# Kernel tuning notes

Hardware: AMD Instinct MI355X
Metric: run time of the kernel (lower is better)

The kernel has to match this reference:

```python
import jax, jax.numpy as jnp
import numpy as np

DIM = 1024
NUM_HEADS = 16
HEAD_DIM = DIM // NUM_HEADS
SCALE = HEAD_DIM ** -0.5


def setup_inputs() -> dict:
    key = jax.random.key(0)
    ks = jax.random.split(key, 7)
    b, n = 2, 2048
    x = jax.random.normal(ks[0], (b, n, DIM), dtype=jnp.float32)
    s = DIM ** -0.5
    Wq = jax.random.normal(ks[1], (DIM, DIM), dtype=jnp.float32) * s
    bq = jax.random.normal(ks[2], (DIM,), dtype=jnp.float32) * 0.01
    Wk = jax.random.normal(ks[3], (DIM, DIM), dtype=jnp.float32) * s
    bk = jax.random.normal(ks[4], (DIM,), dtype=jnp.float32) * 0.01
    Wv = jax.random.normal(ks[5], (DIM, DIM), dtype=jnp.float32) * s
    bv = jax.random.normal(ks[6], (DIM,), dtype=jnp.float32) * 0.01
    return {"x": x, "Wq": Wq, "bq": bq, "Wk": Wk, "bk": bk, "Wv": Wv, "bv": bv}


def reference(x, Wq, bq, Wk, bk, Wv, bv):
    b, n, _ = x.shape
    # Linear projections (torch Linear: x @ W.T + b; here W stored as [in, out])
    q = x @ Wq + bq
    k = x @ Wk + bk
    v = x @ Wv + bv
    # split heads: [b, n, h*d] -> [b, h, n, d]
    split = lambda t: t.reshape(b, n, NUM_HEADS, HEAD_DIM).transpose(0, 2, 1, 3)
    q, k, v = split(q), split(k), split(v)
    sim = jnp.einsum('bhid,bhjd->bhij', q, k) * SCALE
    attn = jax.nn.softmax(sim, axis=-1)
    out = jnp.einsum('bhij,bhjd->bhid', attn, v)
    return out.transpose(0, 2, 1, 3).reshape(b, n, DIM)
```

## Files before the change

kernel.cpp:

```cpp
#include <hip/hip_runtime.h>
#include <cstdint>
#include <cstddef>

#define NB    2
#define SEQ   2048
#define DIMC  1024
#define NH    16
#define HDIM  64
#define MROWS (NB*SEQ)
#define NFEAT (3*DIMC)
#define KVBLK 64

typedef _Float16 half8 __attribute__((ext_vector_type(8)));
typedef _Float16 half4 __attribute__((ext_vector_type(4)));
typedef _Float16 half2v __attribute__((ext_vector_type(2)));
typedef __fp16   fp16x2 __attribute__((ext_vector_type(2)));
typedef float    f32x4 __attribute__((ext_vector_type(4)));

typedef const __attribute__((address_space(1))) void* gas_ptr;
typedef __attribute__((address_space(3))) void*       las_ptr;

__device__ __forceinline__ void gload_lds16(const void* g, void* l) {
    __builtin_amdgcn_global_load_lds((gas_ptr)g, (las_ptr)l, 16, 0, 0);
}

__device__ __forceinline__ float fast_exp2(float x) {
    float r;
    asm("v_exp_f32 %0, %1" : "=v"(r) : "v"(x));
    return r;
}

__device__ __forceinline__ half2v pk_f16(float a, float b) {
    fp16x2 r = __builtin_amdgcn_cvt_pkrtz(a, b);
    return __builtin_bit_cast(half2v, r);
}

__global__ __launch_bounds__(256) void k_prep(const float* __restrict__ x,
                                              const float* __restrict__ Wq,
                                              const float* __restrict__ Wk,
                                              const float* __restrict__ Wv,
                                              _Float16* __restrict__ x16,
                                              _Float16* __restrict__ wt) {
    __shared__ float tile[64][65];
    const int tid = threadIdx.x;
    if (blockIdx.x < 4096) {
        int i = (blockIdx.x * 256 + tid) * 4;
        float4 v = *reinterpret_cast<const float4*>(x + i);
        half4 h = { (_Float16)v.x, (_Float16)v.y, (_Float16)v.z, (_Float16)v.w };
        *reinterpret_cast<half4*>(x16 + i) = h;
        return;
    }
    const int bid  = blockIdx.x - 4096;
    const int midx = bid >> 8;
    const int t2   = bid & 255;
    const int i0   = (t2 >> 4) * 64;
    const int o0   = (t2 & 15) * 64;
    const float* W = (midx == 0) ? Wq : (midx == 1 ? Wk : Wv);
    #pragma unroll
    for (int p = 0; p < 4; ++p) {
        int id = p * 256 + tid;
        int r = id >> 4, c4 = (id & 15) * 4;
        float4 v = *reinterpret_cast<const float4*>(W + (size_t)(i0 + r) * DIMC + o0 + c4);
        tile[r][c4 + 0] = v.x; tile[r][c4 + 1] = v.y;
        tile[r][c4 + 2] = v.z; tile[r][c4 + 3] = v.w;
    }
    __syncthreads();
    #pragma unroll
    for (int p = 0; p < 4; ++p) {
        int id = p * 256 + tid;
        int oc = id >> 4, i4 = (id & 15) * 4;
        half4 h = { (_Float16)tile[i4 + 0][oc], (_Float16)tile[i4 + 1][oc],
                    (_Float16)tile[i4 + 2][oc], (_Float16)tile[i4 + 3][oc] };
        *reinterpret_cast<half4*>(wt + (size_t)(midx * DIMC + o0 + oc) * DIMC + i0 + i4) = h;
    }
}

__global__ __launch_bounds__(512, 2) void k_qkv_gemm(
    const _Float16* __restrict__ x16, const _Float16* __restrict__ wt,
    const float* __restrict__ bq, const float* __restrict__ bk, const float* __restrict__ bv,
    _Float16* __restrict__ q16, _Float16* __restrict__ k16, _Float16* __restrict__ vt16)
{
    __shared__ __align__(16) char lds[131072];
    const int tid = threadIdx.x, lane = tid & 63, w = tid >> 6;
    const int wm = w >> 2, wn = w & 3;
    const int lr = lane & 15, lg = lane >> 4;
    const int swzb = (blockIdx.x & 7) * 24 + (blockIdx.x >> 3);
    const int bn = swzb % (NFEAT / 256);
    const int bm = swzb / (NFEAT / 256);
    const int m0 = bm * 256, n0 = bn * 256;

    const f32x4 zero4 = {0.f, 0.f, 0.f, 0.f};
    f32x4 acc[8][4];
    #pragma unroll
    for (int i = 0; i < 8; ++i)
        #pragma unroll
        for (int j = 0; j < 4; ++j) acc[i][j] = zero4;

    auto stage2 = [&](int buf, int kt, int l) {
        int slot = l * 512 + tid;
        int row  = slot >> 3;
        int cg   = (slot & 7) ^ (row & 7);
        gload_lds16(x16 + (size_t)(m0 + row) * DIMC + kt * 64 + cg * 8,
                    lds + buf * 32768 + slot * 16);
        gload_lds16(wt  + (size_t)(n0 + row) * DIMC + kt * 64 + cg * 8,
                    lds + 65536 + buf * 32768 + slot * 16);
    };

    #pragma unroll
    for (int l = 0; l < 4; ++l) stage2(0, 0, l);

    half8 bf[4][2];
    for (int it = 0; it < 16; ++it) {
        const char* Ab = lds + (it & 1) * 32768;
        const char* Bb = lds + 65536 + (it & 1) * 32768;
        asm volatile("s_waitcnt vmcnt(0)" ::: "memory");
        __builtin_amdgcn_s_barrier();
        #pragma unroll
        for (int p = 0; p < 4; ++p) {
            if (it + 1 < 16) stage2((it + 1) & 1, it + 1, p);
            if (p == 0) {
                #pragma unroll
                for (int nb = 0; nb < 4; ++nb) {
                    int col = wn * 64 + nb * 16 + lr;
                    #pragma unroll
                    for (int kk = 0; kk < 2; ++kk)
                        bf[nb][kk] = *(const half8*)(Bb + col * 128
                                        + (((kk * 4 + lg) ^ (col & 7)) << 4));
                }
            }
            half8 af[2][2];
            #pragma unroll
            for (int m2 = 0; m2 < 2; ++m2) {
                int row = wm * 128 + (p * 2 + m2) * 16 + lr;
                #pragma unroll
                for (int kk = 0; kk < 2; ++kk)
                    af[m2][kk] = *(const half8*)(Ab + row * 128
                                    + (((kk * 4 + lg) ^ (row & 7)) << 4));
            }
            __builtin_amdgcn_s_setprio(1);
            #pragma unroll
            for (int m2 = 0; m2 < 2; ++m2)
                #pragma unroll
                for (int nb = 0; nb < 4; ++nb) {
                    acc[p * 2 + m2][nb] = __builtin_amdgcn_mfma_f32_16x16x32_f16(
                        af[m2][0], bf[nb][0], acc[p * 2 + m2][nb], 0, 0, 0);
                    acc[p * 2 + m2][nb] = __builtin_amdgcn_mfma_f32_16x16x32_f16(
                        af[m2][1], bf[nb][1], acc[p * 2 + m2][nb], 0, 0, 0);
                }
            __builtin_amdgcn_s_setprio(0);
            if (p < 3) __builtin_amdgcn_s_barrier();
        }
    }

    const int sec = n0 >> 10;
    const float* bias = (sec == 0) ? bq : (sec == 1 ? bk : bv);
    const float scl = (sec == 0) ? 0.125f * 1.44269504088896f : 1.0f;
    float bfv[4];
    #pragma unroll
    for (int nb = 0; nb < 4; ++nb)
        bfv[nb] = bias[(n0 & 1023) + wn * 64 + nb * 16 + lr];

    if (sec < 2) {
        _Float16* dst = (sec == 0) ? q16 : k16;
        #pragma unroll
        for (int mb = 0; mb < 8; ++mb)
            #pragma unroll
            for (int i2 = 0; i2 < 4; ++i2) {
                int rg = m0 + wm * 128 + mb * 16 + lg * 4 + i2;
                int bb = rg >> 11, nn = rg & (SEQ - 1);
                #pragma unroll
                for (int nb = 0; nb < 4; ++nb) {
                    int f1 = (n0 & 1023) + wn * 64 + nb * 16 + lr;
                    int hh = f1 >> 6, dd = f1 & 63;
                    dst[((size_t)(bb * NH + hh) * SEQ + nn) * HDIM + dd] =
                        (_Float16)((acc[mb][nb][i2] + bfv[nb]) * scl);
                }
            }
    } else {
        __syncthreads();
        char* lt = lds;
        #pragma unroll
        for (int pass = 0; pass < 2; ++pass) {
            if (wm == pass) {
                #pragma unroll
                for (int mb = 0; mb < 8; ++mb)
                    #pragma unroll
                    for (int nb = 0; nb < 4; ++nb) {
                        int c  = wn * 64 + nb * 16 + lr;
                        int r0 = mb * 16 + lg * 4;
                        half4 hv = { (_Float16)(acc[mb][nb][0] + bfv[nb]),
                                     (_Float16)(acc[mb][nb][1] + bfv[nb]),
                                     (_Float16)(acc[mb][nb][2] + bfv[nb]),
                                     (_Float16)(acc[mb][nb][3] + bfv[nb]) };
                        *(half4*)(lt + c * 272 + r0 * 2) = hv;
                    }
            }
            __syncthreads();
            #pragma unroll
            for (int u = 0; u < 8; ++u) {
                int id = u * 512 + tid;
                int c = id >> 4, r8 = (id & 15) * 8;
                half8 hv = *(const half8*)(lt + c * 272 + r8 * 2);
                int f1 = (n0 & 1023) + c;
                int hh = f1 >> 6, dd = f1 & 63;
                int rg = m0 + pass * 128 + r8;
                int bb = rg >> 11, nn = rg & (SEQ - 1);
                *(half8*)(vt16 + ((size_t)(bb * NH + hh) * HDIM + dd) * SEQ + nn) = hv;
            }
            __syncthreads();
        }
    }
}

__global__ __launch_bounds__(512, 4) void k_attn(
    const _Float16* __restrict__ q16, const _Float16* __restrict__ k16,
    const _Float16* __restrict__ vt16, float* __restrict__ out)
{
    __shared__ __align__(16) char lds[81920];
    const int tid = threadIdx.x, lane = tid & 63, w = tid >> 6;
    const int lr = lane & 15, lg = lane >> 4;
    const int sub = w >> 2;
    const int qg  = w & 3;
    const int swz = (blockIdx.x & 7) * 64 + (blockIdx.x >> 3);
    const int bh = swz >> 4;
    const int qt = swz & 15;
    const int qrow0 = qt * 128 + qg * 32;
    const _Float16* qh = q16 + (size_t)bh * SEQ * HDIM;
    const _Float16* kh = k16 + (size_t)bh * SEQ * HDIM;
    const _Float16* vh = vt16 + (size_t)bh * HDIM * SEQ;
    char* pl = lds + 65536 + w * 2048;
    const int rb = lr >> 3;

    const int srow = tid >> 3;
    const int scg  = (tid & 7) ^ (srow & 7);

    auto stageKV = [&](int buf, int t) {
        const int jA = t * KVBLK, jB = (16 + t) * KVBLK;
        gload_lds16(kh + (size_t)(jA + srow) * HDIM + scg * 8,
                    lds + buf * 8192 + tid * 16);
        gload_lds16(kh + (size_t)(jB + srow) * HDIM + scg * 8,
                    lds + 16384 + buf * 8192 + tid * 16);
        gload_lds16(vh + (size_t)srow * SEQ + jA + scg * 8,
                    lds + 32768 + buf * 8192 + tid * 16);
        gload_lds16(vh + (size_t)srow * SEQ + jB + scg * 8,
                    lds + 49152 + buf * 8192 + tid * 16);
    };

    half8 aq[2][2];
    #pragma unroll
    for (int g = 0; g < 2; ++g)
        #pragma unroll
        for (int kc = 0; kc < 2; ++kc)
            aq[g][kc] = *(const half8*)(qh + (size_t)(qrow0 + g * 16 + lr) * HDIM + kc * 32 + lg * 8);

    const f32x4 zero4 = {0.f, 0.f, 0.f, 0.f};
    f32x4 l4[2] = { zero4, zero4 };
    f32x4 oacc[2][4];
    #pragma unroll
    for (int g = 0; g < 2; ++g)
        #pragma unroll
        for (int i = 0; i < 4; ++i) oacc[g][i] = zero4;

    stageKV(0, 0);
    for (int t = 0; t < 16; ++t) {
        __syncthreads();
        if (t + 1 < 16) stageKV((t + 1) & 1, t + 1);
        const char* Kb = lds + sub * 16384 + (t & 1) * 8192;
        const char* Vb = lds + 32768 + sub * 16384 + (t & 1) * 8192;

        f32x4 s0[4], s1[4];
        __builtin_amdgcn_s_setprio(1);
        #pragma unroll
        for (int jb = 0; jb < 4; ++jb) {
            int row = jb * 16 + lr;
            half8 k0 = *(const half8*)(Kb + row * 128 + (((0 + lg) ^ (row & 7)) << 4));
            half8 k1 = *(const half8*)(Kb + row * 128 + (((4 + lg) ^ (row & 7)) << 4));
            f32x4 a0 = __builtin_amdgcn_mfma_f32_16x16x32_f16(k0, aq[0][0], zero4, 0, 0, 0);
            f32x4 a1 = __builtin_amdgcn_mfma_f32_16x16x32_f16(k0, aq[1][0], zero4, 0, 0, 0);
            a0 = __builtin_amdgcn_mfma_f32_16x16x32_f16(k1, aq[0][1], a0, 0, 0, 0);
            a1 = __builtin_amdgcn_mfma_f32_16x16x32_f16(k1, aq[1][1], a1, 0, 0, 0);
            s0[jb] = a0; s1[jb] = a1;
        }
        __builtin_amdgcn_s_setprio(0);

        #pragma unroll
        for (int jb = 0; jb < 4; ++jb) {
            #pragma unroll
            for (int i = 0; i < 4; ++i) s0[jb][i] = fast_exp2(s0[jb][i]);
            l4[0] += s0[jb];
            half2v w0 = pk_f16(s0[jb][0], s0[jb][1]);
            half2v w1 = pk_f16(s0[jb][2], s0[jb][3]);
            half4 pk = { w0.x, w0.y, w1.x, w1.y };
            *(half4*)(pl + lr * 128 + (((jb * 2 + (lg >> 1)) ^ (lr & 7)) << 4)
                      + (((lg & 1) ^ rb) << 3)) = pk;
        }
        half4 pk1[4];
        #pragma unroll
        for (int jb = 0; jb < 4; ++jb) {
            #pragma unroll
            for (int i = 0; i < 4; ++i) s1[jb][i] = fast_exp2(s1[jb][i]);
            l4[1] += s1[jb];
            half2v w0 = pk_f16(s1[jb][0], s1[jb][1]);
            half2v w1 = pk_f16(s1[jb][2], s1[jb][3]);
            pk1[jb] = half4{ w0.x, w0.y, w1.x, w1.y };
        }
        asm volatile("s_waitcnt lgkmcnt(0)" ::: "memory");
        const char* prow = pl + lr * 128;
        half8 ap[2][2];
        {
            half4 l0 = *(const half4*)(prow + (((0 + lg) ^ (lr & 7)) << 4) + (rb << 3));
            half4 h0 = *(const half4*)(prow + (((0 + lg) ^ (lr & 7)) << 4) + ((1 ^ rb) << 3));
            half4 l1 = *(const half4*)(prow + (((4 + lg) ^ (lr & 7)) << 4) + (rb << 3));
            half4 h1 = *(const half4*)(prow + (((4 + lg) ^ (lr & 7)) << 4) + ((1 ^ rb) << 3));
            ap[0][0] = half8{ l0.x, l0.y, l0.z, l0.w, h0.x, h0.y, h0.z, h0.w };
            ap[0][1] = half8{ l1.x, l1.y, l1.z, l1.w, h1.x, h1.y, h1.z, h1.w };
        }
        #pragma unroll
        for (int jb = 0; jb < 4; ++jb)
            *(half4*)(pl + lr * 128 + (((jb * 2 + (lg >> 1)) ^ (lr & 7)) << 4)
                      + (((lg & 1) ^ rb) << 3)) = pk1[jb];
        asm volatile("s_waitcnt lgkmcnt(0)" ::: "memory");
        {
            half4 l0 = *(const half4*)(prow + (((0 + lg) ^ (lr & 7)) << 4) + (rb << 3));
            half4 h0 = *(const half4*)(prow + (((0 + lg) ^ (lr & 7)) << 4) + ((1 ^ rb) << 3));
            half4 l1 = *(const half4*)(prow + (((4 + lg) ^ (lr & 7)) << 4) + (rb << 3));
            half4 h1 = *(const half4*)(prow + (((4 + lg) ^ (lr & 7)) << 4) + ((1 ^ rb) << 3));
            ap[1][0] = half8{ l0.x, l0.y, l0.z, l0.w, h0.x, h0.y, h0.z, h0.w };
            ap[1][1] = half8{ l1.x, l1.y, l1.z, l1.w, h1.x, h1.y, h1.z, h1.w };
        }
        __builtin_amdgcn_s_setprio(1);
        #pragma unroll
        for (int db = 0; db < 4; ++db) {
            int row = db * 16 + lr;
            half8 vf0 = *(const half8*)(Vb + row * 128 + (((0 + lg) ^ (row & 7)) << 4));
            half8 vf1 = *(const half8*)(Vb + row * 128 + (((4 + lg) ^ (row & 7)) << 4));
            oacc[0][db] = __builtin_amdgcn_mfma_f32_16x16x32_f16(ap[0][0], vf0, oacc[0][db], 0, 0, 0);
            oacc[1][db] = __builtin_amdgcn_mfma_f32_16x16x32_f16(ap[1][0], vf0, oacc[1][db], 0, 0, 0);
            oacc[0][db] = __builtin_amdgcn_mfma_f32_16x16x32_f16(ap[0][1], vf1, oacc[0][db], 0, 0, 0);
            oacc[1][db] = __builtin_amdgcn_mfma_f32_16x16x32_f16(ap[1][1], vf1, oacc[1][db], 0, 0, 0);
        }
        __builtin_amdgcn_s_setprio(0);
    }

    __syncthreads();
    char* xch = lds;
    if (sub == 1) {
        char* sl = xch + (qg * 2) * 5120;
        #pragma unroll
        for (int g = 0; g < 2; ++g) {
            #pragma unroll
            for (int db = 0; db < 4; ++db)
                *(f32x4*)(sl + g * 5120 + db * 1024 + lane * 16) = oacc[g][db];
            *(f32x4*)(sl + g * 5120 + 4096 + lane * 16) = l4[g];
        }
    }
    __syncthreads();
    if (sub == 0) {
        char* sl = xch + (qg * 2) * 5120;
        #pragma unroll
        for (int g = 0; g < 2; ++g) {
            #pragma unroll
            for (int db = 0; db < 4; ++db)
                oacc[g][db] += *(const f32x4*)(sl + g * 5120 + db * 1024 + lane * 16);
            l4[g] += *(const f32x4*)(sl + g * 5120 + 4096 + lane * 16);
        }
        const int bb = bh >> 4, hh = bh & 15;
        #pragma unroll
        for (int g = 0; g < 2; ++g) {
            float l_i = (l4[g][0] + l4[g][1]) + (l4[g][2] + l4[g][3]);
            l_i += __shfl_xor(l_i, 16);
            l_i += __shfl_xor(l_i, 32);
            float rlq[4];
            #pragma unroll
            for (int i = 0; i < 4; ++i)
                rlq[i] = 1.0f / __shfl(l_i, lg * 4 + i);
            #pragma unroll
            for (int db = 0; db < 4; ++db)
                #pragma unroll
                for (int i = 0; i < 4; ++i) {
                    int nn = qrow0 + g * 16 + lg * 4 + i;
                    out[((size_t)bb * SEQ + nn) * DIMC + hh * HDIM + db * 16 + lr] =
                        oacc[g][db][i] * rlq[i];
                }
        }
    }
}

extern "C" void kernel_launch(void* const* d_in, const int* in_sizes, int n_in,
                              void* d_out, int out_size, void* d_ws, size_t ws_size,
                              hipStream_t stream)
{
    const float* x  = (const float*)d_in[0];
    const float* Wq = (const float*)d_in[1];
    const float* bq = (const float*)d_in[2];
    const float* Wk = (const float*)d_in[3];
    const float* bk = (const float*)d_in[4];
    const float* Wv = (const float*)d_in[5];
    const float* bv = (const float*)d_in[6];
    float* out = (float*)d_out;

    char* ws = (char*)d_ws;
    _Float16* x16  = (_Float16*)ws;
    _Float16* wt   = (_Float16*)(ws + ((size_t)8  << 20));
    _Float16* q16  = (_Float16*)(ws + ((size_t)14 << 20));
    _Float16* k16  = (_Float16*)(ws + ((size_t)22 << 20));
    _Float16* vt16 = (_Float16*)(ws + ((size_t)30 << 20));

    k_prep<<<4096 + 768, 256, 0, stream>>>(x, Wq, Wk, Wv, x16, wt);
    k_qkv_gemm<<<(MROWS / 256) * (NFEAT / 256), 512, 0, stream>>>(x16, wt, bq, bk, bv,
                                                                  q16, k16, vt16);
    k_attn<<<32 * (SEQ / 128), 512, 0, stream>>>(q16, k16, vt16, out);
}
```

Baseline: 84.38 us.

## Fuse fp32-to-fp16 conversion of x into QKV GEMM operand staging

```diff
diff --git a/kernel.cpp b/kernel.cpp
--- a/kernel.cpp
+++ b/kernel.cpp
@@ -35,22 +35,13 @@
     return __builtin_bit_cast(half2v, r);
 }
 
-__global__ __launch_bounds__(256) void k_prep(const float* __restrict__ x,
-                                              const float* __restrict__ Wq,
+__global__ __launch_bounds__(256) void k_prep(const float* __restrict__ Wq,
                                               const float* __restrict__ Wk,
                                               const float* __restrict__ Wv,
-                                              _Float16* __restrict__ x16,
                                               _Float16* __restrict__ wt) {
     __shared__ float tile[64][65];
     const int tid = threadIdx.x;
-    if (blockIdx.x < 4096) {
-        int i = (blockIdx.x * 256 + tid) * 4;
-        float4 v = *reinterpret_cast<const float4*>(x + i);
-        half4 h = { (_Float16)v.x, (_Float16)v.y, (_Float16)v.z, (_Float16)v.w };
-        *reinterpret_cast<half4*>(x16 + i) = h;
-        return;
-    }
-    const int bid  = blockIdx.x - 4096;
+    const int bid  = blockIdx.x;
     const int midx = bid >> 8;
     const int t2   = bid & 255;
     const int i0   = (t2 >> 4) * 64;
@@ -76,7 +67,7 @@
 }
 
 __global__ __launch_bounds__(512, 2) void k_qkv_gemm(
-    const _Float16* __restrict__ x16, const _Float16* __restrict__ wt,
+    const float* __restrict__ xf, const _Float16* __restrict__ wt,
     const float* __restrict__ bq, const float* __restrict__ bk, const float* __restrict__ bv,
     _Float16* __restrict__ q16, _Float16* __restrict__ k16, _Float16* __restrict__ vt16)
 {
@@ -96,28 +87,57 @@
         #pragma unroll
         for (int j = 0; j < 4; ++j) acc[i][j] = zero4;
 
-    auto stage2 = [&](int buf, int kt, int l) {
-        int slot = l * 512 + tid;
-        int row  = slot >> 3;
-        int cg   = (slot & 7) ^ (row & 7);
-        gload_lds16(x16 + (size_t)(m0 + row) * DIMC + kt * 64 + cg * 8,
-                    lds + buf * 32768 + slot * 16);
-        gload_lds16(wt  + (size_t)(n0 + row) * DIMC + kt * 64 + cg * 8,
-                    lds + 65536 + buf * 32768 + slot * 16);
+    float4 va[4][2];
+
+    auto aload = [&](int kt) {
+        #pragma unroll
+        for (int l = 0; l < 4; ++l) {
+            int slot = l * 512 + tid;
+            int row  = slot >> 3;
+            int cg   = (slot & 7) ^ (row & 7);
+            const float* p = xf + (size_t)(m0 + row) * DIMC + kt * 64 + cg * 8;
+            va[l][0] = *reinterpret_cast<const float4*>(p);
+            va[l][1] = *reinterpret_cast<const float4*>(p + 4);
+        }
     };
-
-    #pragma unroll
-    for (int l = 0; l < 4; ++l) stage2(0, 0, l);
+    auto astore = [&](int buf) {
+        #pragma unroll
+        for (int l = 0; l < 4; ++l) {
+            int slot = l * 512 + tid;
+            half8 hv = { (_Float16)va[l][0].x, (_Float16)va[l][0].y,
+                         (_Float16)va[l][0].z, (_Float16)va[l][0].w,
+                         (_Float16)va[l][1].x, (_Float16)va[l][1].y,
+                         (_Float16)va[l][1].z, (_Float16)va[l][1].w };
+            *(half8*)(lds + buf * 32768 + slot * 16) = hv;
+        }
+    };
+    auto bstage = [&](int buf, int kt) {
+        #pragma unroll
+        for (int l = 0; l < 4; ++l) {
+            int slot = l * 512 + tid;
+            int row  = slot >> 3;
+            int cg   = (slot & 7) ^ (row & 7);
+            gload_lds16(wt + (size_t)(n0 + row) * DIMC + kt * 64 + cg * 8,
+                        lds + 65536 + buf * 32768 + slot * 16);
+        }
+    };
+
+    aload(0); astore(0); bstage(0, 0);
 
     half8 bf[4][2];
     for (int it = 0; it < 16; ++it) {
         const char* Ab = lds + (it & 1) * 32768;
         const char* Bb = lds + 65536 + (it & 1) * 32768;
-        asm volatile("s_waitcnt vmcnt(0)" ::: "memory");
+        asm volatile("s_waitcnt vmcnt(0) lgkmcnt(0)" ::: "memory");
         __builtin_amdgcn_s_barrier();
         #pragma unroll
         for (int p = 0; p < 4; ++p) {
-            if (it + 1 < 16) stage2((it + 1) & 1, it + 1, p);
+            if (p == 0 && it + 1 < 16) {
+                aload(it + 1);
+                bstage((it + 1) & 1, it + 1);
+            }
+            if (p == 2 && it + 1 < 16)
+                astore((it + 1) & 1);
             if (p == 0) {
                 #pragma unroll
                 for (int nb = 0; nb < 4; ++nb) {
@@ -400,14 +420,13 @@
     float* out = (float*)d_out;
 
     char* ws = (char*)d_ws;
-    _Float16* x16  = (_Float16*)ws;
     _Float16* wt   = (_Float16*)(ws + ((size_t)8  << 20));
     _Float16* q16  = (_Float16*)(ws + ((size_t)14 << 20));
     _Float16* k16  = (_Float16*)(ws + ((size_t)22 << 20));
     _Float16* vt16 = (_Float16*)(ws + ((size_t)30 << 20));
 
-    k_prep<<<4096 + 768, 256, 0, stream>>>(x, Wq, Wk, Wv, x16, wt);
-    k_qkv_gemm<<<(MROWS / 256) * (NFEAT / 256), 512, 0, stream>>>(x16, wt, bq, bk, bv,
+    k_prep<<<768, 256, 0, stream>>>(Wq, Wk, Wv, wt);
+    k_qkv_gemm<<<(MROWS / 256) * (NFEAT / 256), 512, 0, stream>>>(x, wt, bq, bk, bv,
                                                                   q16, k16, vt16);
     k_attn<<<32 * (SEQ / 128), 512, 0, stream>>>(q16, k16, vt16, out);
 }
```

New measurement: 96.83 us. 14.7% more time.
